# Kernel tuning notes

Measured on AMD Instinct MI355X. Metric: run time of the kernel, lower is better.

Reference implementation:

```python
import jax, jax.numpy as jnp
import numpy as np

B_SZ, L, H, D, N, R, K = 2, 1024, 2048, 4096, 16, 128, 4


def setup_inputs() -> dict:
    key = jax.random.key(0)
    ks = jax.random.split(key, 10)
    s = lambda *sh: 1.0 / np.sqrt(sh[-1])
    inp = {
        "hidden_states": jax.random.normal(ks[0], (B_SZ, L, H), jnp.float32),
        "in_proj_w": jax.random.normal(ks[1], (2 * D, H), jnp.float32) * s(H),
        "conv_w": jax.random.normal(ks[2], (D, 1, K), jnp.float32) * s(K),
        "conv_b": jax.random.normal(ks[3], (D,), jnp.float32) * 0.02,
        "x_proj_w": jax.random.normal(ks[4], (R + 2 * N, D), jnp.float32) * s(D),
        "dt_proj_w": jax.random.normal(ks[5], (D, R), jnp.float32) * s(R),
        "dt_proj_b": jax.random.normal(ks[6], (D,), jnp.float32) * 0.02,
        # A_log = log(arange(1, N+1)) broadcast over D, as in the module init
        "A_log": jnp.broadcast_to(jnp.log(jnp.arange(1, N + 1, dtype=jnp.float32))[None, :], (D, N)),
        "D_param": jnp.ones((D,), jnp.float32),
        "out_proj_w": jax.random.normal(ks[7], (H, D), jnp.float32) * s(D),
    }
    return inp


def _mamba_forward(hidden_states, in_proj_w, conv_w, conv_b, x_proj_w,
                   dt_proj_w, dt_proj_b, A_log, D_param, out_proj_w):
    silu = jax.nn.silu
    # in_proj: [B,L,H] @ [H,2D] -> [B,L,2D] -> [B,2D,L]
    proj = jnp.einsum("blh,ph->bpl", hidden_states, in_proj_w)
    u, gate = jnp.split(proj, 2, axis=1)  # each [B,D,L]
    # depthwise causal conv1d (padding K-1 on the left, then first L outputs)
    u = jax.lax.conv_general_dilated(
        u, conv_w, window_strides=(1,), padding=[(K - 1, 0)],
        dimension_numbers=("NCH", "OIH", "NCH"), feature_group_count=D,
    ) + conv_b[None, :, None]
    u = silu(u)  # [B,D,L]
    # x_proj on [B,L,D]
    ssm_params = jnp.einsum("bdl,pd->blp", u, x_proj_w)  # [B,L,R+2N]
    time_step, Bmat, Cmat = jnp.split(ssm_params, [R, R + N], axis=-1)
    # dt_proj + softplus -> [B,D,L]
    dt = jnp.einsum("blr,dr->bld", time_step, dt_proj_w) + dt_proj_b
    dt = jax.nn.softplus(dt).transpose(0, 2, 1)  # [B,D,L]
    A = -jnp.exp(A_log)  # [D,N]

    # selective scan over time; carry ssm_state [B,D,N]
    def step(state, xs):
        dt_t, B_t, C_t, u_t = xs  # [B,D],[B,N],[B,N],[B,D]
        dA = jnp.exp(A[None] * dt_t[:, :, None])          # [B,D,N]
        dBu = dt_t[:, :, None] * B_t[:, None, :] * u_t[:, :, None]
        state = dA * state + dBu
        y_t = jnp.einsum("bdn,bn->bd", state, C_t)        # [B,D]
        return state, y_t

    xs = (dt.transpose(2, 0, 1),          # [L,B,D]
          Bmat.transpose(1, 0, 2),        # [L,B,N]
          Cmat.transpose(1, 0, 2),        # [L,B,N]
          u.transpose(2, 0, 1))           # [L,B,D]
    init = jnp.zeros((hidden_states.shape[0], D, N), hidden_states.dtype)
    _, ys = jax.lax.scan(step, init, xs)   # ys [L,B,D]
    y = ys.transpose(1, 2, 0)              # [B,D,L]
    y = y + u * D_param[None, :, None]
    y = y * silu(gate)
    # out_proj: [B,L,D] @ [D,H]
    return jnp.einsum("bdl,hd->blh", y, out_proj_w)


def reference(hidden_states, in_proj_w, conv_w, conv_b, x_proj_w,
              dt_proj_w, dt_proj_b, A_log, D_param, out_proj_w):
    return _mamba_forward(hidden_states, in_proj_w, conv_w, conv_b, x_proj_w,
                          dt_proj_w, dt_proj_b, A_log, D_param, out_proj_w)
```

## Files before the change

kernel.cpp:

```cpp
#include <hip/hip_runtime.h>

#define L_SEQ 1024
#define DD 4096
#define NC 32
#define CT 32

typedef short bf16x8 __attribute__((ext_vector_type(8)));
typedef float f32x4 __attribute__((ext_vector_type(4)));
typedef unsigned short u16;

typedef const __attribute__((address_space(1))) void gas_t;
typedef __attribute__((address_space(3))) void las_t;

__device__ inline u16 f2bf(float f) {
  unsigned int u = __float_as_uint(f);
  u = (u + 0x7FFFu + ((u >> 16) & 1u)) >> 16;
  return (u16)u;
}

__device__ inline float bf2f(u16 v) {
  return __uint_as_float(((unsigned int)v) << 16);
}

__device__ inline float softplusf(float x) {
  return x > 20.f ? x : log1pf(expf(x));
}

__global__ __launch_bounds__(256) void cast_all_k(
    const float* __restrict__ hs, const float* __restrict__ w_in,
    const float* __restrict__ xw, const float* __restrict__ dtw,
    const float* __restrict__ ow, u16* __restrict__ hs_bf,
    u16* __restrict__ win_bf, u16* __restrict__ xw_bf,
    u16* __restrict__ dtw_bf, u16* __restrict__ ow_bf) {
  const int blk = blockIdx.x;
  const float* s;
  u16* d;
  int base;
  if (blk < 4096)        { s = hs;   d = hs_bf;  base = blk; }
  else if (blk < 20480)  { s = w_in; d = win_bf; base = blk - 4096; }
  else if (blk < 21120)  { s = xw;   d = xw_bf;  base = blk - 20480; }
  else if (blk < 21632)  { s = dtw;  d = dtw_bf; base = blk - 21120; }
  else                   { s = ow;   d = ow_bf;  base = blk - 21632; }
  const int i = (base * 256 + threadIdx.x) * 4;
  float4 v = *(const float4*)(s + i);
  ushort4 o;
  o.x = f2bf(v.x); o.y = f2bf(v.y); o.z = f2bf(v.z); o.w = f2bf(v.w);
  *(ushort4*)(d + i) = o;
}

__global__ __launch_bounds__(256) void reduce4_k(const float* __restrict__ p,
                                                 float* __restrict__ out,
                                                 long n) {
  long i = ((long)blockIdx.x * 256 + threadIdx.x) * 4;
  if (i >= n) return;
  float4 a = *(const float4*)(p + i);
  float4 b = *(const float4*)(p + n + i);
  float4 c = *(const float4*)(p + 2 * n + i);
  float4 d = *(const float4*)(p + 3 * n + i);
  float4 o;
  o.x = (a.x + b.x) + (c.x + d.x);
  o.y = (a.y + b.y) + (c.y + d.y);
  o.z = (a.z + b.z) + (c.z + d.z);
  o.w = (a.w + b.w) + (c.w + d.w);
  *(float4*)(out + i) = o;
}

__global__ __launch_bounds__(256) void xproj_fin_k(const float* __restrict__ parts,
                                                   u16* __restrict__ ts,
                                                   float* __restrict__ ssm) {
  const int idx = blockIdx.x * 256 + threadIdx.x;
  float s = 0.f;
#pragma unroll
  for (int z = 0; z < 8; z++) s += parts[z * 327680 + idx];
  const int row = idx / 160;
  const int col = idx - row * 160;
  if (col < 128) ts[row * 128 + col] = f2bf(s);
  else ssm[idx] = s;
}

template <int CMODE, bool SWZ>
__global__ __launch_bounds__(512, 2) void gemm256(const u16* __restrict__ A,
                                                  const u16* __restrict__ B,
                                                  void* __restrict__ Cv,
                                                  int Nld, int K, int kc,
                                                  long zstride) {
  __shared__ u16 lds[2][2][8192];
  const int tid = threadIdx.x;
  const int lane = tid & 63, wid = tid >> 6;
  const int wm = wid >> 2, wn = wid & 3;
  int ty = blockIdx.y, tx = blockIdx.x;
  if (SWZ) {
    int flat = blockIdx.y * 32 + blockIdx.x;
    int xcd = flat & 7, pos = flat >> 3;
    ty = (xcd & 1) * 4 + (pos >> 3);
    tx = (xcd >> 1) * 8 + (pos & 7);
  }
  const long tm = (long)ty * 256, tn = (long)tx * 256;

  const long ks0 = (CMODE == 2) ? (long)blockIdx.z * kc : 0;

  const int srow = tid >> 2;
  const int sks = (((tid & 3) ^ ((srow >> 1) & 3))) * 8;
  const u16* gA0 = A + (tm + srow) * (long)K + ks0 + sks;
  const u16* gA1 = A + (tm + 128 + srow) * (long)K + ks0 + sks;
  const u16* gB0 = B + (tn + srow) * (long)K + ks0 + sks;
  const u16* gB1 = B + (tn + 128 + srow) * (long)K + ks0 + sks;
  const int sb0 = wid * 512;
  const int sb1 = 4096 + wid * 512;

  f32x4 acc[8][4] = {};

  const int lr = lane & 15, kq = lane >> 4;
  const int arow = wm * 128 + lr;
  const int brow = wn * 64 + lr;
  const int granA = (kq ^ ((arow >> 1) & 3)) * 8;
  const int granB = (kq ^ ((brow >> 1) & 3)) * 8;

  const int KT = kc >> 5;
  int cur = 0;
  __builtin_amdgcn_global_load_lds((gas_t*)gA0, (las_t*)&lds[0][0][sb0], 16, 0, 0);
  __builtin_amdgcn_global_load_lds((gas_t*)gA1, (las_t*)&lds[0][0][sb1], 16, 0, 0);
  __builtin_amdgcn_global_load_lds((gas_t*)gB0, (las_t*)&lds[0][1][sb0], 16, 0, 0);
  __builtin_amdgcn_global_load_lds((gas_t*)gB1, (las_t*)&lds[0][1][sb1], 16, 0, 0);
  __syncthreads();

  for (int kt = 0; kt < KT; ++kt) {
    if (kt + 1 < KT) {
      const long ko = (long)(kt + 1) << 5;
      const int nb = cur ^ 1;
      __builtin_amdgcn_global_load_lds((gas_t*)(gA0 + ko), (las_t*)&lds[nb][0][sb0], 16, 0, 0);
      __builtin_amdgcn_global_load_lds((gas_t*)(gA1 + ko), (las_t*)&lds[nb][0][sb1], 16, 0, 0);
      __builtin_amdgcn_global_load_lds((gas_t*)(gB0 + ko), (las_t*)&lds[nb][1][sb0], 16, 0, 0);
      __builtin_amdgcn_global_load_lds((gas_t*)(gB1 + ko), (las_t*)&lds[nb][1][sb1], 16, 0, 0);
    }
    bf16x8 af[8], bfr[4];
#pragma unroll
    for (int n = 0; n < 4; n++)
      bfr[n] = *(const bf16x8*)&lds[cur][1][(brow + n * 16) * 32 + granB];
#pragma unroll
    for (int m = 0; m < 8; m++)
      af[m] = *(const bf16x8*)&lds[cur][0][(arow + m * 16) * 32 + granA];
#pragma unroll
    for (int m = 0; m < 8; m++)
#pragma unroll
      for (int n = 0; n < 4; n++)
        acc[m][n] = __builtin_amdgcn_mfma_f32_16x16x32_bf16(af[m], bfr[n],
                                                            acc[m][n], 0, 0, 0);
    __syncthreads();
    cur ^= 1;
  }

  float* Cf = (CMODE == 2) ? (float*)Cv + (long)blockIdx.z * zstride
                           : (float*)Cv;

  const int rg = (lane >> 4) * 4;
#pragma unroll
  for (int m = 0; m < 8; m++) {
    const long gr = tm + wm * 128 + m * 16 + rg;
#pragma unroll
    for (int n = 0; n < 4; n++) {
      const long gc = tn + wn * 64 + n * 16 + lr;
#pragma unroll
      for (int r = 0; r < 4; r++) {
        if (CMODE == 1)
          ((u16*)Cv)[(gr + r) * (long)Nld + gc] = f2bf(acc[m][n][r]);
        else
          Cf[(gr + r) * (long)Nld + gc] = acc[m][n][r];
      }
    }
  }
}

template <bool CLAMP_N, int MODE>
__global__ __launch_bounds__(256) void gemm_bt(const u16* __restrict__ A,
                                               const u16* __restrict__ B,
                                               void* __restrict__ Cv,
                                               const float* __restrict__ ebias,
                                               int Nv, int K, int ldc, int kc,
                                               long zs) {
  __shared__ u16 lA[128 * 32];
  __shared__ u16 lB[128 * 32];
  const int tid = threadIdx.x;
  const int lane = tid & 63, wid = tid >> 6;
  const int wm = wid >> 1, wn = wid & 1;
  const long tm = (long)blockIdx.y * 128, tn = (long)blockIdx.x * 128;

  f32x4 acc[4][4] = {};

  const int roff = lane >> 2;
  const int sks = (((lane & 3) ^ ((roff >> 1) & 3))) * 8;
  const int c0 = wid * 2, c1 = c0 + 1;
  const long ra0 = tm + c0 * 16 + roff;
  const long ra1 = tm + c1 * 16 + roff;
  long rb0 = tn + c0 * 16 + roff;
  long rb1 = tn + c1 * 16 + roff;
  if (CLAMP_N) {
    if (rb0 >= Nv) rb0 = Nv - 1;
    if (rb1 >= Nv) rb1 = Nv - 1;
  }
  const u16* gA0 = A + ra0 * K + sks;
  const u16* gA1 = A + ra1 * K + sks;
  const u16* gB0 = B + rb0 * K + sks;
  const u16* gB1 = B + rb1 * K + sks;
  u16* sA0 = &lA[c0 * 512];
  u16* sA1 = &lA[c1 * 512];
  u16* sB0 = &lB[c0 * 512];
  u16* sB1 = &lB[c1 * 512];

  int ks0 = 0, ks1 = K;
  if (MODE == 2) { ks0 = blockIdx.z * kc; ks1 = ks0 + kc; }

  const int lr = lane & 15, kq = lane >> 4;
  const int arow = wm * 64 + lr, brow = wn * 64 + lr;
  const int granA = (kq ^ ((arow >> 1) & 3)) * 8;
  const int granB = (kq ^ ((brow >> 1) & 3)) * 8;

  for (int ks = ks0; ks < ks1; ks += 32) {
    __builtin_amdgcn_global_load_lds((gas_t*)(gA0 + ks), (las_t*)sA0, 16, 0, 0);
    __builtin_amdgcn_global_load_lds((gas_t*)(gA1 + ks), (las_t*)sA1, 16, 0, 0);
    __builtin_amdgcn_global_load_lds((gas_t*)(gB0 + ks), (las_t*)sB0, 16, 0, 0);
    __builtin_amdgcn_global_load_lds((gas_t*)(gB1 + ks), (las_t*)sB1, 16, 0, 0);
    __syncthreads();
    bf16x8 af[4], bfr[4];
#pragma unroll
    for (int i = 0; i < 4; i++) {
      af[i]  = *(const bf16x8*)&lA[(arow + i * 16) * 32 + granA];
      bfr[i] = *(const bf16x8*)&lB[(brow + i * 16) * 32 + granB];
    }
#pragma unroll
    for (int i = 0; i < 4; i++)
#pragma unroll
      for (int j = 0; j < 4; j++)
        acc[i][j] = __builtin_amdgcn_mfma_f32_16x16x32_bf16(af[i], bfr[j],
                                                            acc[i][j], 0, 0, 0);
    __syncthreads();
  }

  float* Cf = (MODE == 2) ? (float*)Cv + (long)blockIdx.z * zs : (float*)Cv;

  const int rg = (lane >> 4) * 4;
#pragma unroll
  for (int i = 0; i < 4; i++) {
    const long gr = tm + wm * 64 + i * 16 + rg;
#pragma unroll
    for (int j = 0; j < 4; j++) {
      const long gc = tn + wn * 64 + j * 16 + lr;
      if (CLAMP_N && gc >= Nv) continue;
      float bias = 0.f;
      if (MODE == 1) bias = ebias[gc];
#pragma unroll
      for (int r = 0; r < 4; r++) {
        float v = acc[i][j][r];
        if (MODE == 1)
          ((u16*)Cv)[(gr + r) * (long)ldc + gc] = f2bf(softplusf(v + bias));
        else
          Cf[(gr + r) * (long)ldc + gc] = v;
      }
    }
  }
}

__global__ __launch_bounds__(256) void conv_silu_k(const u16* __restrict__ projb,
                                                   const float* __restrict__ cw,
                                                   const float* __restrict__ cb,
                                                   u16* __restrict__ ub) {
  const int idx = blockIdx.x * 256 + threadIdx.x;
  const int d = idx & (DD - 1);
  const int bl = idx >> 12;
  const int l = bl & (L_SEQ - 1);
  const float4 w = *(const float4*)(cw + d * 4);
  float s = cb[d];
  const u16* pp = projb + (long)bl * 8192 + d;
  s += w.w * bf2f(pp[0]);
  if (l >= 1) s += w.z * bf2f(pp[-8192]);
  if (l >= 2) s += w.y * bf2f(pp[-2 * 8192]);
  if (l >= 3) s += w.x * bf2f(pp[-3 * 8192]);
  const float r = s / (1.f + expf(-s));
  ub[idx] = f2bf(r);
}

__global__ __launch_bounds__(256) void scan_p1(const u16* __restrict__ dt,
                                               const u16* __restrict__ u,
                                               const float* __restrict__ ssm,
                                               const float* __restrict__ A_log,
                                               float* __restrict__ Sbuf,
                                               float* __restrict__ Pbuf) {
  __shared__ float sBC[CT * 32];
  __shared__ u16 dtl[CT][256];
  __shared__ u16 ul[CT][256];
  const int tid = threadIdx.x;
  const int d0 = blockIdx.x * 256;
  const int d = d0 + tid;
  const int c = blockIdx.y, b = blockIdx.z;
  const long blbase = (long)b * L_SEQ + (long)c * CT;
  for (int i = tid; i < CT * 32; i += 256) {
    int tt = i >> 5, j = i & 31;
    sBC[i] = ssm[(blbase + tt) * 160 + 128 + j];
  }
  const u16* dtg = dt + blbase * DD + d0;
  const u16* ug  = u  + blbase * DD + d0;
#pragma unroll
  for (int it = 0; it < 4; ++it) {
    const int ck = it * 256 + tid;
    const int row = ck >> 5, ch = (ck & 31) * 8;
    *(uint4*)&dtl[row][ch] = *(const uint4*)(dtg + (long)row * DD + ch);
    *(uint4*)&ul[row][ch]  = *(const uint4*)(ug  + (long)row * DD + ch);
  }
  __syncthreads();
  float a2[16], st[16], pr[16];
#pragma unroll
  for (int g = 0; g < 4; g++) {
    float4 al = *(const float4*)(A_log + d * 16 + g * 4);
    a2[g*4+0] = -expf(al.x) * 1.4426950408889634f;
    a2[g*4+1] = -expf(al.y) * 1.4426950408889634f;
    a2[g*4+2] = -expf(al.z) * 1.4426950408889634f;
    a2[g*4+3] = -expf(al.w) * 1.4426950408889634f;
  }
#pragma unroll
  for (int n = 0; n < 16; n++) { st[n] = 0.f; pr[n] = 1.f; }
  for (int tt = 0; tt < CT; tt++) {
    const float dtv = bf2f(dtl[tt][tid]);
    const float uv = bf2f(ul[tt][tid]);
    const float dtu = dtv * uv;
    const float4* Bv = (const float4*)&sBC[tt * 32];
#pragma unroll
    for (int g = 0; g < 4; g++) {
      const float4 Bg = Bv[g];
      float e;
      e = exp2f(a2[g*4+0]*dtv); st[g*4+0] = e*st[g*4+0] + dtu*Bg.x; pr[g*4+0] *= e;
      e = exp2f(a2[g*4+1]*dtv); st[g*4+1] = e*st[g*4+1] + dtu*Bg.y; pr[g*4+1] *= e;
      e = exp2f(a2[g*4+2]*dtv); st[g*4+2] = e*st[g*4+2] + dtu*Bg.z; pr[g*4+2] *= e;
      e = exp2f(a2[g*4+3]*dtv); st[g*4+3] = e*st[g*4+3] + dtu*Bg.w; pr[g*4+3] *= e;
    }
  }
  const long base = (((long)b * NC + c) * DD + d) * 16;
#pragma unroll
  for (int g = 0; g < 4; g++) {
    *(float4*)(Sbuf + base + g * 4) = make_float4(st[g*4+0], st[g*4+1], st[g*4+2], st[g*4+3]);
    *(float4*)(Pbuf + base + g * 4) = make_float4(pr[g*4+0], pr[g*4+1], pr[g*4+2], pr[g*4+3]);
  }
}

__global__ __launch_bounds__(256) void scan_p2(const float* __restrict__ Sbuf,
                                               const float* __restrict__ Pbuf,
                                               float* __restrict__ carry) {
  const int idx = blockIdx.x * 256 + threadIdx.x;
  const int ng = idx & 3;
  const int d = (idx >> 2) & (DD - 1);
  const int b = idx >> 14;
  const long stride = (long)DD * 16;
  long base = ((long)b * NC * DD + d) * 16 + ng * 4;
  float4 P = *(const float4*)(Pbuf + base);
  float4 S = *(const float4*)(Sbuf + base);
  float4 cr = make_float4(0.f, 0.f, 0.f, 0.f);
  for (int c = 0; c < NC; c++) {
    float4 Pn, Sn;
    if (c + 1 < NC) {
      Pn = *(const float4*)(Pbuf + base + stride);
      Sn = *(const float4*)(Sbuf + base + stride);
    }
    *(float4*)(carry + base) = cr;
    cr.x = P.x * cr.x + S.x;
    cr.y = P.y * cr.y + S.y;
    cr.z = P.z * cr.z + S.z;
    cr.w = P.w * cr.w + S.w;
    P = Pn; S = Sn;
    base += stride;
  }
}

__global__ __launch_bounds__(256) void scan_p3(const u16* __restrict__ dt,
                                               const u16* __restrict__ u,
                                               const float* __restrict__ ssm,
                                               const u16* __restrict__ projb,
                                               const float* __restrict__ A_log,
                                               const float* __restrict__ Dp,
                                               const float* __restrict__ carry,
                                               u16* __restrict__ yb) {
  __shared__ float sBC[CT * 32];
  __shared__ u16 dtl[CT][256];
  __shared__ u16 ul[CT][256];
  const int tid = threadIdx.x;
  const int d0 = blockIdx.x * 256;
  const int d = d0 + tid;
  const int c = blockIdx.y, b = blockIdx.z;
  const long blbase = (long)b * L_SEQ + (long)c * CT;
  for (int i = tid; i < CT * 32; i += 256) {
    int tt = i >> 5, j = i & 31;
    sBC[i] = ssm[(blbase + tt) * 160 + 128 + j];
  }
  const u16* dtg = dt + blbase * DD + d0;
  const u16* ug  = u  + blbase * DD + d0;
#pragma unroll
  for (int it = 0; it < 4; ++it) {
    const int ck = it * 256 + tid;
    const int row = ck >> 5, ch = (ck & 31) * 8;
    *(uint4*)&dtl[row][ch] = *(const uint4*)(dtg + (long)row * DD + ch);
    *(uint4*)&ul[row][ch]  = *(const uint4*)(ug  + (long)row * DD + ch);
  }
  __syncthreads();
  float a2[16], st[16];
#pragma unroll
  for (int g = 0; g < 4; g++) {
    float4 al = *(const float4*)(A_log + d * 16 + g * 4);
    a2[g*4+0] = -expf(al.x) * 1.4426950408889634f;
    a2[g*4+1] = -expf(al.y) * 1.4426950408889634f;
    a2[g*4+2] = -expf(al.z) * 1.4426950408889634f;
    a2[g*4+3] = -expf(al.w) * 1.4426950408889634f;
  }
  const long cbase = (((long)b * NC + c) * DD + d) * 16;
#pragma unroll
  for (int g = 0; g < 4; g++) {
    float4 cv = *(const float4*)(carry + cbase + g * 4);
    st[g*4+0] = cv.x; st[g*4+1] = cv.y; st[g*4+2] = cv.z; st[g*4+3] = cv.w;
  }
  const float dp = Dp[d];
  const u16* gp = projb + blbase * 8192 + DD + d;
  u16 gnext = gp[0];
  for (int tt = 0; tt < CT; tt++) {
    const u16 gcur = gnext;
    if (tt + 1 < CT) gnext = gp[(tt + 1) * 8192];
    const float dtv = bf2f(dtl[tt][tid]);
    const float uv = bf2f(ul[tt][tid]);
    const float dtu = dtv * uv;
    float acc = 0.f;
    const float4* Bv = (const float4*)&sBC[tt * 32];
    const float4* Cv = Bv + 4;
#pragma unroll
    for (int g = 0; g < 4; g++) {
      const float4 Bg = Bv[g];
      const float4 Cg = Cv[g];
      float e;
      e = exp2f(a2[g*4+0]*dtv); st[g*4+0] = e*st[g*4+0] + dtu*Bg.x; acc += st[g*4+0]*Cg.x;
      e = exp2f(a2[g*4+1]*dtv); st[g*4+1] = e*st[g*4+1] + dtu*Bg.y; acc += st[g*4+1]*Cg.y;
      e = exp2f(a2[g*4+2]*dtv); st[g*4+2] = e*st[g*4+2] + dtu*Bg.z; acc += st[g*4+2]*Cg.z;
      e = exp2f(a2[g*4+3]*dtv); st[g*4+3] = e*st[g*4+3] + dtu*Bg.w; acc += st[g*4+3]*Cg.w;
    }
    const float g = bf2f(gcur);
    const float yv = (acc + uv * dp) * (g / (1.f + expf(-g)));
    yb[(blbase + tt) * DD + d] = f2bf(yv);
  }
}

extern "C" void kernel_launch(void* const* d_in, const int* in_sizes, int n_in,
                              void* d_out, int out_size, void* d_ws, size_t ws_size,
                              hipStream_t stream) {
  const float* hs     = (const float*)d_in[0];
  const float* w_in   = (const float*)d_in[1];
  const float* conv_w = (const float*)d_in[2];
  const float* conv_b = (const float*)d_in[3];
  const float* xw     = (const float*)d_in[4];
  const float* dtw    = (const float*)d_in[5];
  const float* dtb    = (const float*)d_in[6];
  const float* A_log  = (const float*)d_in[7];
  const float* Dp     = (const float*)d_in[8];
  const float* ow     = (const float*)d_in[9];
  float* out = (float*)d_out;

  constexpr size_t SZ_HS_BF  = 2048ull * 2048 * 2;
  constexpr size_t SZ_WIN_BF = 8192ull * 2048 * 2;
  constexpr size_t SZ_PROJ   = 2048ull * 8192 * 2;
  constexpr size_t SZ_UBF    = 2048ull * 4096 * 2;
  constexpr size_t SZ_XW_BF  = 160ull * 4096 * 2;
  constexpr size_t SZ_SSM    = 2048ull * 160 * 4;
  constexpr size_t SZ_TS_BF  = 2048ull * 128 * 2;
  constexpr size_t SZ_DTW_BF = 4096ull * 128 * 2;
  constexpr size_t SZ_DT     = 2048ull * 4096 * 2;
  constexpr size_t SZ_OW_BF  = 2048ull * 4096 * 2;
  constexpr size_t SZ_YBF    = 2048ull * 4096 * 2;
  constexpr size_t SZ_SCAN   = 2ull * NC * DD * 16 * 4;
  constexpr size_t SZ_PXP    = 8ull * 2048 * 160 * 4;
  constexpr size_t TOTAL = SZ_HS_BF + SZ_WIN_BF + SZ_PROJ + SZ_UBF +
                           SZ_XW_BF + SZ_SSM + SZ_TS_BF + SZ_DTW_BF + SZ_DT +
                           SZ_OW_BF + SZ_YBF + 3 * SZ_SCAN + SZ_PXP;
  if (ws_size < TOTAL) return;

  char* w = (char*)d_ws;
  u16* hs_bf   = (u16*)w;   w += SZ_HS_BF;
  u16* win_bf  = (u16*)w;   w += SZ_WIN_BF;
  u16* projb   = (u16*)w;   w += SZ_PROJ;
  u16* u_bf    = (u16*)w;   w += SZ_UBF;
  u16* xw_bf   = (u16*)w;   w += SZ_XW_BF;
  float* ssm   = (float*)w; w += SZ_SSM;
  u16* ts_bf   = (u16*)w;   w += SZ_TS_BF;
  u16* dtw_bf  = (u16*)w;   w += SZ_DTW_BF;
  u16* dt_bf   = (u16*)w;   w += SZ_DT;
  u16* ow_bf   = (u16*)w;   w += SZ_OW_BF;
  u16* y_bf    = (u16*)w;   w += SZ_YBF;
  float* Sbuf  = (float*)w; w += SZ_SCAN;
  float* Pbuf  = (float*)w; w += SZ_SCAN;
  float* carry = (float*)w; w += SZ_SCAN;
  float* partsx = (float*)w; w += SZ_PXP;

  float* parts = (float*)win_bf;

  cast_all_k<<<29824, 256, 0, stream>>>(hs, w_in, xw, dtw, ow,
                                        hs_bf, win_bf, xw_bf, dtw_bf, ow_bf);

  gemm256<1, true><<<dim3(32, 8), 512, 0, stream>>>(
      hs_bf, win_bf, projb, 8192, 2048, 2048, 0);

  conv_silu_k<<<32768, 256, 0, stream>>>(projb, conv_w, conv_b, u_bf);

  gemm_bt<true, 2><<<dim3(2, 16, 8), 256, 0, stream>>>(
      u_bf, xw_bf, partsx, nullptr, 160, 4096, 160, 512, 327680);

  xproj_fin_k<<<1280, 256, 0, stream>>>(partsx, ts_bf, ssm);

  gemm_bt<false, 1><<<dim3(32, 16), 256, 0, stream>>>(
      ts_bf, dtw_bf, dt_bf, dtb, 4096, 128, 4096, 0, 0);

  scan_p1<<<dim3(16, NC, 2), 256, 0, stream>>>(dt_bf, u_bf, ssm, A_log, Sbuf, Pbuf);
  scan_p2<<<128, 256, 0, stream>>>(Sbuf, Pbuf, carry);
  scan_p3<<<dim3(16, NC, 2), 256, 0, stream>>>(dt_bf, u_bf, ssm, projb, A_log, Dp,
                                               carry, y_bf);

  gemm256<2, false><<<dim3(8, 8, 4), 512, 0, stream>>>(
      y_bf, ow_bf, parts, 2048, 4096, 1024, 2048ll * 2048);
  reduce4_k<<<4096, 256, 0, stream>>>(parts, out, 2048ll * 2048);
}
```

Baseline: 355.4 us.

## Triple-buffer GEMM pipeline, vectorize conv, bf16 split-K partials, deeper x_proj split

The 256x256 GEMM moves from double to triple buffering, with explicit vmcnt waits and raw barriers so the global-to-LDS loads for three k-steps run ahead of the MFMAs. The conv+SiLU kernel now handles 8 channels per thread with 128-bit loads and stores. The out_proj split-K partials are stored as bf16, halving the partial write and the reduce read at some cost in precision. The x_proj split-K goes from 8 to 16 slices and reuses the scan buffer as its workspace, which removes a dedicated allocation.

Measured after the change: 356.0 us. About the same (+0.2%).

```diff
diff --git a/kernel.cpp b/kernel.cpp
--- a/kernel.cpp
+++ b/kernel.cpp
@@ -48,21 +48,25 @@
   *(ushort4*)(d + i) = o;
 }
 
-__global__ __launch_bounds__(256) void reduce4_k(const float* __restrict__ p,
-                                                 float* __restrict__ out,
-                                                 long n) {
-  long i = ((long)blockIdx.x * 256 + threadIdx.x) * 4;
+__global__ __launch_bounds__(256) void reduce4b_k(const u16* __restrict__ p,
+                                                  float* __restrict__ out,
+                                                  long n) {
+  long i = ((long)blockIdx.x * 256 + threadIdx.x) * 8;
   if (i >= n) return;
-  float4 a = *(const float4*)(p + i);
-  float4 b = *(const float4*)(p + n + i);
-  float4 c = *(const float4*)(p + 2 * n + i);
-  float4 d = *(const float4*)(p + 3 * n + i);
-  float4 o;
-  o.x = (a.x + b.x) + (c.x + d.x);
-  o.y = (a.y + b.y) + (c.y + d.y);
-  o.z = (a.z + b.z) + (c.z + d.z);
-  o.w = (a.w + b.w) + (c.w + d.w);
-  *(float4*)(out + i) = o;
+  uint4 a = *(const uint4*)(p + i);
+  uint4 b = *(const uint4*)(p + n + i);
+  uint4 c = *(const uint4*)(p + 2 * n + i);
+  uint4 d = *(const uint4*)(p + 3 * n + i);
+  const u16* qa = (const u16*)&a;
+  const u16* qb = (const u16*)&b;
+  const u16* qc = (const u16*)&c;
+  const u16* qd = (const u16*)&d;
+  float o[8];
+#pragma unroll
+  for (int j = 0; j < 8; j++)
+    o[j] = (bf2f(qa[j]) + bf2f(qb[j])) + (bf2f(qc[j]) + bf2f(qd[j]));
+  *(float4*)(out + i) = make_float4(o[0], o[1], o[2], o[3]);
+  *(float4*)(out + i + 4) = make_float4(o[4], o[5], o[6], o[7]);
 }
 
 __global__ __launch_bounds__(256) void xproj_fin_k(const float* __restrict__ parts,
@@ -71,7 +75,7 @@
   const int idx = blockIdx.x * 256 + threadIdx.x;
   float s = 0.f;
 #pragma unroll
-  for (int z = 0; z < 8; z++) s += parts[z * 327680 + idx];
+  for (int z = 0; z < 16; z++) s += parts[z * 327680 + idx];
   const int row = idx / 160;
   const int col = idx - row * 160;
   if (col < 128) ts[row * 128 + col] = f2bf(s);
@@ -84,7 +88,7 @@
                                                   void* __restrict__ Cv,
                                                   int Nld, int K, int kc,
                                                   long zstride) {
-  __shared__ u16 lds[2][2][8192];
+  __shared__ u16 lds[3][2][8192];
   const int tid = threadIdx.x;
   const int lane = tid & 63, wid = tid >> 6;
   const int wm = wid >> 2, wn = wid & 3;
@@ -117,41 +121,53 @@
   const int granB = (kq ^ ((brow >> 1) & 3)) * 8;
 
   const int KT = kc >> 5;
-  int cur = 0;
-  __builtin_amdgcn_global_load_lds((gas_t*)gA0, (las_t*)&lds[0][0][sb0], 16, 0, 0);
-  __builtin_amdgcn_global_load_lds((gas_t*)gA1, (las_t*)&lds[0][0][sb1], 16, 0, 0);
-  __builtin_amdgcn_global_load_lds((gas_t*)gB0, (las_t*)&lds[0][1][sb0], 16, 0, 0);
-  __builtin_amdgcn_global_load_lds((gas_t*)gB1, (las_t*)&lds[0][1][sb1], 16, 0, 0);
-  __syncthreads();
-
+
+#define STG(buf, kt)                                                           \
+  {                                                                            \
+    const long ko_ = (long)(kt) << 5;                                          \
+    __builtin_amdgcn_global_load_lds((gas_t*)(gA0 + ko_),                      \
+                                     (las_t*)&lds[buf][0][sb0], 16, 0, 0);     \
+    __builtin_amdgcn_global_load_lds((gas_t*)(gA1 + ko_),                      \
+                                     (las_t*)&lds[buf][0][sb1], 16, 0, 0);     \
+    __builtin_amdgcn_global_load_lds((gas_t*)(gB0 + ko_),                      \
+                                     (las_t*)&lds[buf][1][sb0], 16, 0, 0);     \
+    __builtin_amdgcn_global_load_lds((gas_t*)(gB1 + ko_),                      \
+                                     (las_t*)&lds[buf][1][sb1], 16, 0, 0);     \
+  }
+
+  STG(0, 0);
+  STG(1, 1);
+  STG(2, 2);
+
+  int buf = 0;
   for (int kt = 0; kt < KT; ++kt) {
-    if (kt + 1 < KT) {
-      const long ko = (long)(kt + 1) << 5;
-      const int nb = cur ^ 1;
-      __builtin_amdgcn_global_load_lds((gas_t*)(gA0 + ko), (las_t*)&lds[nb][0][sb0], 16, 0, 0);
-      __builtin_amdgcn_global_load_lds((gas_t*)(gA1 + ko), (las_t*)&lds[nb][0][sb1], 16, 0, 0);
-      __builtin_amdgcn_global_load_lds((gas_t*)(gB0 + ko), (las_t*)&lds[nb][1][sb0], 16, 0, 0);
-      __builtin_amdgcn_global_load_lds((gas_t*)(gB1 + ko), (las_t*)&lds[nb][1][sb1], 16, 0, 0);
-    }
+    if (kt + 3 <= KT)
+      asm volatile("s_waitcnt vmcnt(8)" ::: "memory");
+    else if (kt + 2 == KT)
+      asm volatile("s_waitcnt vmcnt(4)" ::: "memory");
+    else
+      asm volatile("s_waitcnt vmcnt(0)" ::: "memory");
+    __builtin_amdgcn_s_barrier();
+
     bf16x8 af[8], bfr[4];
 #pragma unroll
     for (int n = 0; n < 4; n++)
-      bfr[n] = *(const bf16x8*)&lds[cur][1][(brow + n * 16) * 32 + granB];
+      bfr[n] = *(const bf16x8*)&lds[buf][1][(brow + n * 16) * 32 + granB];
 #pragma unroll
     for (int m = 0; m < 8; m++)
-      af[m] = *(const bf16x8*)&lds[cur][0][(arow + m * 16) * 32 + granA];
+      af[m] = *(const bf16x8*)&lds[buf][0][(arow + m * 16) * 32 + granA];
 #pragma unroll
     for (int m = 0; m < 8; m++)
 #pragma unroll
       for (int n = 0; n < 4; n++)
         acc[m][n] = __builtin_amdgcn_mfma_f32_16x16x32_bf16(af[m], bfr[n],
                                                             acc[m][n], 0, 0, 0);
-    __syncthreads();
-    cur ^= 1;
-  }
-
-  float* Cf = (CMODE == 2) ? (float*)Cv + (long)blockIdx.z * zstride
-                           : (float*)Cv;
+    asm volatile("s_waitcnt lgkmcnt(0)" ::: "memory");
+    __builtin_amdgcn_s_barrier();
+    if (kt + 3 < KT) STG(buf, kt + 3);
+    buf = (buf == 2) ? 0 : buf + 1;
+  }
+#undef STG
 
   const int rg = (lane >> 4) * 4;
 #pragma unroll
@@ -165,7 +181,8 @@
         if (CMODE == 1)
           ((u16*)Cv)[(gr + r) * (long)Nld + gc] = f2bf(acc[m][n][r]);
         else
-          Cf[(gr + r) * (long)Nld + gc] = acc[m][n][r];
+          ((u16*)Cv)[(long)blockIdx.z * zstride + (gr + r) * (long)Nld + gc] =
+              f2bf(acc[m][n][r]);
       }
     }
   }
@@ -264,19 +281,37 @@
                                                    const float* __restrict__ cw,
                                                    const float* __restrict__ cb,
                                                    u16* __restrict__ ub) {
-  const int idx = blockIdx.x * 256 + threadIdx.x;
-  const int d = idx & (DD - 1);
-  const int bl = idx >> 12;
+  const int gid = blockIdx.x * 256 + threadIdx.x;
+  const int d = (gid & 511) * 8;
+  const int bl = gid >> 9;
   const int l = bl & (L_SEQ - 1);
-  const float4 w = *(const float4*)(cw + d * 4);
-  float s = cb[d];
   const u16* pp = projb + (long)bl * 8192 + d;
-  s += w.w * bf2f(pp[0]);
-  if (l >= 1) s += w.z * bf2f(pp[-8192]);
-  if (l >= 2) s += w.y * bf2f(pp[-2 * 8192]);
-  if (l >= 3) s += w.x * bf2f(pp[-3 * 8192]);
-  const float r = s / (1.f + expf(-s));
-  ub[idx] = f2bf(r);
+  const uint4 zero = make_uint4(0, 0, 0, 0);
+  uint4 t0 = *(const uint4*)pp;
+  uint4 t1 = (l >= 1) ? *(const uint4*)(pp - 8192) : zero;
+  uint4 t2 = (l >= 2) ? *(const uint4*)(pp - 16384) : zero;
+  uint4 t3 = (l >= 3) ? *(const uint4*)(pp - 24576) : zero;
+  const u16* q0 = (const u16*)&t0;
+  const u16* q1 = (const u16*)&t1;
+  const u16* q2 = (const u16*)&t2;
+  const u16* q3 = (const u16*)&t3;
+  float4 b0 = *(const float4*)(cb + d);
+  float4 b1 = *(const float4*)(cb + d + 4);
+  const float* bb = &b0.x;
+  u16 ov[8];
+#pragma unroll
+  for (int j = 0; j < 8; j++) {
+    const float4 w = *(const float4*)(cw + (d + j) * 4);
+    float s = (j < 4) ? ((const float*)&b0)[j] : ((const float*)&b1)[j - 4];
+    s += w.w * bf2f(q0[j]);
+    s += w.z * bf2f(q1[j]);
+    s += w.y * bf2f(q2[j]);
+    s += w.x * bf2f(q3[j]);
+    const float r = s / (1.f + expf(-s));
+    ov[j] = f2bf(r);
+  }
+  (void)bb;
+  *(uint4*)(ub + (long)bl * DD + d) = *(uint4*)ov;
 }
 
 __global__ __launch_bounds__(256) void scan_p1(const u16* __restrict__ dt,
@@ -469,10 +504,9 @@
   constexpr size_t SZ_OW_BF  = 2048ull * 4096 * 2;
   constexpr size_t SZ_YBF    = 2048ull * 4096 * 2;
   constexpr size_t SZ_SCAN   = 2ull * NC * DD * 16 * 4;
-  constexpr size_t SZ_PXP    = 8ull * 2048 * 160 * 4;
   constexpr size_t TOTAL = SZ_HS_BF + SZ_WIN_BF + SZ_PROJ + SZ_UBF +
                            SZ_XW_BF + SZ_SSM + SZ_TS_BF + SZ_DTW_BF + SZ_DT +
-                           SZ_OW_BF + SZ_YBF + 3 * SZ_SCAN + SZ_PXP;
+                           SZ_OW_BF + SZ_YBF + 3 * SZ_SCAN;
   if (ws_size < TOTAL) return;
 
   char* w = (char*)d_ws;
@@ -490,9 +524,9 @@
   float* Sbuf  = (float*)w; w += SZ_SCAN;
   float* Pbuf  = (float*)w; w += SZ_SCAN;
   float* carry = (float*)w; w += SZ_SCAN;
-  float* partsx = (float*)w; w += SZ_PXP;
-
-  float* parts = (float*)win_bf;
+
+  float* partsx = Sbuf;
+  u16* parts = win_bf;
 
   cast_all_k<<<29824, 256, 0, stream>>>(hs, w_in, xw, dtw, ow,
                                         hs_bf, win_bf, xw_bf, dtw_bf, ow_bf);
@@ -500,10 +534,10 @@
   gemm256<1, true><<<dim3(32, 8), 512, 0, stream>>>(
       hs_bf, win_bf, projb, 8192, 2048, 2048, 0);
 
-  conv_silu_k<<<32768, 256, 0, stream>>>(projb, conv_w, conv_b, u_bf);
-
-  gemm_bt<true, 2><<<dim3(2, 16, 8), 256, 0, stream>>>(
-      u_bf, xw_bf, partsx, nullptr, 160, 4096, 160, 512, 327680);
+  conv_silu_k<<<4096, 256, 0, stream>>>(projb, conv_w, conv_b, u_bf);
+
+  gemm_bt<true, 2><<<dim3(2, 16, 16), 256, 0, stream>>>(
+      u_bf, xw_bf, partsx, nullptr, 160, 4096, 160, 256, 327680);
 
   xproj_fin_k<<<1280, 256, 0, stream>>>(partsx, ts_bf, ssm);
 
@@ -517,5 +551,5 @@
 
   gemm256<2, false><<<dim3(8, 8, 4), 512, 0, stream>>>(
       y_bf, ow_bf, parts, 2048, 4096, 1024, 2048ll * 2048);
-  reduce4_k<<<4096, 256, 0, stream>>>(parts, out, 2048ll * 2048);
-}
+  reduce4b_k<<<2048, 256, 0, stream>>>(parts, out, 2048ll * 2048);
+}
```
